# Performance work log

Measured on AMD Instinct MI355X. Metric: run time of the kernel, lower is better.

The kernel has to match this reference:

```python
import jax, jax.numpy as jnp
import numpy as np

B, N, E = 64, 256, 8192


def setup_inputs() -> dict:
    key = jax.random.key(0)
    k1, k2, k3, k4, k5 = jax.random.split(key, 5)
    P = jax.random.uniform(k1, (B, N, N), dtype=jnp.float32)
    d_error = jax.random.uniform(k2, (N, N), dtype=jnp.float32)
    edge_i = jax.random.randint(k3, (B, E), 0, N, dtype=jnp.int32)
    edge_j = jax.random.randint(k4, (B, E), 0, N, dtype=jnp.int32)
    edge_w = jax.random.uniform(k5, (B, E), dtype=jnp.float32)
    return {"P": P, "d_error": d_error, "edge_i": edge_i,
            "edge_j": edge_j, "edge_w": edge_w}


def reference(P, d_error, edge_i, edge_j, edge_w):
    # cost_e = P[b, i_e, :] @ d_error @ P[b, j_e, :]
    # Precompute Q = P @ d_error once, then gather per edge (memory-bound).
    Q = jnp.einsum('bin,nm->bim', P, d_error)            # [B, N, N]
    Qi = jnp.take_along_axis(Q, edge_i[:, :, None], axis=1)   # [B, E, N]
    Pj = jnp.take_along_axis(P, edge_j[:, :, None], axis=1)   # [B, E, N]
    cost = jnp.sum(Qi * Pj, axis=-1)                      # [B, E]
    sample_loss = jnp.sum(edge_w * cost, axis=-1)         # [B]
    sample_weight = jnp.maximum(jnp.sum(edge_w, axis=-1), 1e-8)
    # every sample has edges -> valid_samples == B, i.e. a mean over batch
    return jnp.mean(sample_loss / sample_weight)
```

## Files before the change

### kernel.cpp

```cpp
#include <hip/hip_runtime.h>

#define NN 256
#define BB 64
#define EE 8192

typedef __attribute__((ext_vector_type(8))) short bf16x8;
typedef __attribute__((ext_vector_type(8))) unsigned short u16x8;
typedef __attribute__((ext_vector_type(4))) float f32x4;

__device__ __forceinline__ unsigned short f2bf(float f) {
  union { float f; unsigned u; } x; x.f = f;
  unsigned r = x.u + 0x7FFFu + ((x.u >> 16) & 1u);
  return (unsigned short)(r >> 16);
}

__device__ __forceinline__ float bf2f(unsigned short h) {
  union { unsigned u; float f; } x; x.u = ((unsigned)h) << 16;
  return x.f;
}

__global__ __launch_bounds__(256) void convertP(const float* __restrict__ P,
                                                unsigned short* __restrict__ Pbf) {
  int idx = blockIdx.x * 256 + threadIdx.x;
  float4 v = ((const float4*)P)[idx];
  ushort4 o;
  o.x = f2bf(v.x); o.y = f2bf(v.y); o.z = f2bf(v.z); o.w = f2bf(v.w);
  ((ushort4*)Pbf)[idx] = o;
}

__global__ __launch_bounds__(256) void transposeD(const float* __restrict__ D,
                                                  unsigned short* __restrict__ Dt) {
  __shared__ float t[32][33];
  int bx = blockIdx.x & 7;
  int by = blockIdx.x >> 3;
  int c = threadIdx.x & 31, r0 = threadIdx.x >> 5;
#pragma unroll
  for (int p = 0; p < 4; ++p) {
    int row = r0 + p * 8;
    t[row][c] = D[(bx * 32 + row) * NN + by * 32 + c];
  }
  __syncthreads();
#pragma unroll
  for (int p = 0; p < 4; ++p) {
    int row = r0 + p * 8;
    Dt[(by * 32 + row) * NN + bx * 32 + c] = f2bf(t[c][row]);
  }
}

__device__ __forceinline__ void gemm_mainloop(const unsigned short* __restrict__ Ag,
                                              const unsigned short* __restrict__ Bg,
                                              int rowBase, int colBase,
                                              unsigned short* As, unsigned short* Bs,
                                              f32x4 acc[4][4]) {
  const int tid = threadIdx.x;
  const int lane = tid & 63;
  const int wave = tid >> 6;
  const int wr = (wave >> 1) * 64;
  const int wc = (wave & 1) * 64;
  const int frm = lane & 15;
  const int fq = (lane >> 4) * 8;

  for (int ks = 0; ks < 8; ++ks) {
    const int k0 = ks * 32;
    __syncthreads();
#pragma unroll
    for (int i = 0; i < 2; ++i) {
      int c = i * 256 + tid;
      int row = c >> 2;
      int col = (c & 3) * 8;
      u16x8 va = *(const u16x8*)(Ag + (rowBase + row) * NN + k0 + col);
      u16x8 vb = *(const u16x8*)(Bg + (colBase + row) * NN + k0 + col);
      *(u16x8*)(As + c * 8) = va;
      *(u16x8*)(Bs + c * 8) = vb;
    }
    __syncthreads();
    bf16x8 af[4], bfr[4];
#pragma unroll
    for (int t = 0; t < 4; ++t) {
      af[t]  = *(const bf16x8*)(As + (wr + t * 16 + frm) * 32 + fq);
      bfr[t] = *(const bf16x8*)(Bs + (wc + t * 16 + frm) * 32 + fq);
    }
#pragma unroll
    for (int tr = 0; tr < 4; ++tr)
#pragma unroll
      for (int tc = 0; tc < 4; ++tc)
        acc[tr][tc] = __builtin_amdgcn_mfma_f32_16x16x32_bf16(af[tr], bfr[tc],
                                                              acc[tr][tc], 0, 0, 0);
  }
}

__global__ __launch_bounds__(256) void gemm1(const unsigned short* __restrict__ Pbf,
                                             const unsigned short* __restrict__ Dt,
                                             unsigned short* __restrict__ Qbf) {
  __shared__ __align__(16) unsigned short As[4096];
  __shared__ __align__(16) unsigned short Bs[4096];
  int b = blockIdx.x >> 2;
  int tile = blockIdx.x & 3;
  int ty = tile >> 1, tx = tile & 1;
  f32x4 acc[4][4];
#pragma unroll
  for (int i = 0; i < 4; ++i)
#pragma unroll
    for (int j = 0; j < 4; ++j) acc[i][j] = (f32x4){0.f, 0.f, 0.f, 0.f};

  gemm_mainloop(Pbf + b * NN * NN, Dt, ty * 128, tx * 128, As, Bs, acc);

  const int lane = threadIdx.x & 63;
  const int wave = threadIdx.x >> 6;
  const int wr = (wave >> 1) * 64, wc = (wave & 1) * 64;
  unsigned short* outB = Qbf + b * NN * NN;
#pragma unroll
  for (int tr = 0; tr < 4; ++tr)
#pragma unroll
    for (int tc = 0; tc < 4; ++tc)
#pragma unroll
      for (int r = 0; r < 4; ++r) {
        int rg = ty * 128 + wr + tr * 16 + (lane >> 4) * 4 + r;
        int cg = tx * 128 + wc + tc * 16 + (lane & 15);
        outB[rg * NN + cg] = f2bf(acc[tr][tc][r]);
      }
}

__global__ __launch_bounds__(256) void gemm2_fused(const unsigned short* __restrict__ Qbf,
                                                   const unsigned short* __restrict__ Pbf,
                                                   const int* __restrict__ ei,
                                                   const int* __restrict__ ej,
                                                   const float* __restrict__ ew,
                                                   float* __restrict__ loss_part,
                                                   float* __restrict__ w_part) {
  __shared__ __align__(16) unsigned short As[4096];
  __shared__ __align__(16) unsigned short Bs[4096];
  __shared__ __align__(16) unsigned short Mt[128 * 130];
  __shared__ float red[8];
  int b = blockIdx.x >> 2;
  int tile = blockIdx.x & 3;
  int ty = tile >> 1, tx = tile & 1;
  f32x4 acc[4][4];
#pragma unroll
  for (int i = 0; i < 4; ++i)
#pragma unroll
    for (int j = 0; j < 4; ++j) acc[i][j] = (f32x4){0.f, 0.f, 0.f, 0.f};

  gemm_mainloop(Qbf + b * NN * NN, Pbf + b * NN * NN, ty * 128, tx * 128, As, Bs, acc);

  const int tid = threadIdx.x;
  const int lane = tid & 63;
  const int wave = tid >> 6;
  const int wr = (wave >> 1) * 64, wc = (wave & 1) * 64;
#pragma unroll
  for (int tr = 0; tr < 4; ++tr)
#pragma unroll
    for (int tc = 0; tc < 4; ++tc)
#pragma unroll
      for (int r = 0; r < 4; ++r) {
        int rl = wr + tr * 16 + (lane >> 4) * 4 + r;
        int cl = wc + tc * 16 + (lane & 15);
        Mt[rl * 130 + cl] = f2bf(acc[tr][tc][r]);
      }
  __syncthreads();

  float lsum = 0.f, wsum = 0.f;
  const int r0 = ty * 128, c0 = tx * 128;
  const int eb = b * EE;
#pragma unroll 4
  for (int s = 0; s < 32; ++s) {
    int e = eb + s * 256 + tid;
    int i = ei[e], j = ej[e];
    float w = ew[e];
    wsum += w;
    int il = i - r0, jl = j - c0;
    if (((unsigned)il < 128u) && ((unsigned)jl < 128u))
      lsum += w * bf2f(Mt[il * 130 + jl]);
  }
#pragma unroll
  for (int o = 32; o; o >>= 1) {
    lsum += __shfl_down(lsum, o);
    wsum += __shfl_down(wsum, o);
  }
  if (lane == 0) { red[wave] = lsum; red[4 + wave] = wsum; }
  __syncthreads();
  if (tid == 0) {
    loss_part[b * 4 + tile] = red[0] + red[1] + red[2] + red[3];
    if (tile == 0) w_part[b] = red[4] + red[5] + red[6] + red[7];
  }
}

__global__ void finalize(const float* __restrict__ loss_part,
                         const float* __restrict__ w_part,
                         float* __restrict__ out) {
  int b = threadIdx.x;
  float l = loss_part[b * 4] + loss_part[b * 4 + 1] +
            loss_part[b * 4 + 2] + loss_part[b * 4 + 3];
  float w = w_part[b];
  float r = l / fmaxf(w, 1e-8f);
#pragma unroll
  for (int o = 32; o; o >>= 1) r += __shfl_down(r, o);
  if (b == 0) out[0] = r * (1.0f / 64.0f);
}

extern "C" void kernel_launch(void* const* d_in, const int* in_sizes, int n_in,
                              void* d_out, int out_size, void* d_ws, size_t ws_size,
                              hipStream_t stream) {
  const float* P  = (const float*)d_in[0];
  const float* D  = (const float*)d_in[1];
  const int*   ei = (const int*)d_in[2];
  const int*   ej = (const int*)d_in[3];
  const float* ew = (const float*)d_in[4];
  float* out = (float*)d_out;

  char* ws = (char*)d_ws;
  unsigned short* Pbf = (unsigned short*)ws;
  unsigned short* Qbf = (unsigned short*)(ws + 8388608);
  unsigned short* Dt  = (unsigned short*)(ws + 16777216);
  float* loss_part    = (float*)(ws + 16908288);
  float* w_part       = (float*)(ws + 16909312);

  convertP<<<4096, 256, 0, stream>>>(P, Pbf);
  transposeD<<<64, 256, 0, stream>>>(D, Dt);
  gemm1<<<256, 256, 0, stream>>>(Pbf, Dt, Qbf);
  gemm2_fused<<<256, 256, 0, stream>>>(Qbf, Pbf, ei, ej, ew, loss_part, w_part);
  finalize<<<1, 64, 0, stream>>>(loss_part, w_part, out);
}
```

Before: 105.4 us.

## Fuse P bf16 conversion into GEMM loaders with register prefetch and atomic finalize

Removes the separate fp32-to-bf16 conversion kernel for P and instead converts while staging tiles in both GEMM kernels, which now read fp32 P directly. The k-loop adds register prefetching of the next tile so global loads overlap MFMA work. The finalize kernel is replaced by a per-block atomicAdd into a zeroed output, and edge loads are vectorized to int2/float2. The trade-off is reading fp32 P twice instead of bf16 P, plus nondeterministic float atomic summation order.

After: 102.5 us. -2.7%, faster.

```diff
diff --git a/kernel.cpp b/kernel.cpp
--- a/kernel.cpp
+++ b/kernel.cpp
@@ -17,15 +17,6 @@
 __device__ __forceinline__ float bf2f(unsigned short h) {
   union { unsigned u; float f; } x; x.u = ((unsigned)h) << 16;
   return x.f;
-}
-
-__global__ __launch_bounds__(256) void convertP(const float* __restrict__ P,
-                                                unsigned short* __restrict__ Pbf) {
-  int idx = blockIdx.x * 256 + threadIdx.x;
-  float4 v = ((const float4*)P)[idx];
-  ushort4 o;
-  o.x = f2bf(v.x); o.y = f2bf(v.y); o.z = f2bf(v.z); o.w = f2bf(v.w);
-  ((ushort4*)Pbf)[idx] = o;
 }
 
 __global__ __launch_bounds__(256) void transposeD(const float* __restrict__ D,
@@ -47,67 +38,78 @@
   }
 }
 
-__device__ __forceinline__ void gemm_mainloop(const unsigned short* __restrict__ Ag,
-                                              const unsigned short* __restrict__ Bg,
-                                              int rowBase, int colBase,
-                                              unsigned short* As, unsigned short* Bs,
-                                              f32x4 acc[4][4]) {
-  const int tid = threadIdx.x;
-  const int lane = tid & 63;
-  const int wave = tid >> 6;
-  const int wr = (wave >> 1) * 64;
-  const int wc = (wave & 1) * 64;
-  const int frm = lane & 15;
-  const int fq = (lane >> 4) * 8;
-
-  for (int ks = 0; ks < 8; ++ks) {
-    const int k0 = ks * 32;
-    __syncthreads();
-#pragma unroll
-    for (int i = 0; i < 2; ++i) {
-      int c = i * 256 + tid;
-      int row = c >> 2;
-      int col = (c & 3) * 8;
-      u16x8 va = *(const u16x8*)(Ag + (rowBase + row) * NN + k0 + col);
-      u16x8 vb = *(const u16x8*)(Bg + (colBase + row) * NN + k0 + col);
-      *(u16x8*)(As + c * 8) = va;
-      *(u16x8*)(Bs + c * 8) = vb;
-    }
-    __syncthreads();
-    bf16x8 af[4], bfr[4];
-#pragma unroll
-    for (int t = 0; t < 4; ++t) {
-      af[t]  = *(const bf16x8*)(As + (wr + t * 16 + frm) * 32 + fq);
-      bfr[t] = *(const bf16x8*)(Bs + (wc + t * 16 + frm) * 32 + fq);
-    }
-#pragma unroll
-    for (int tr = 0; tr < 4; ++tr)
-#pragma unroll
-      for (int tc = 0; tc < 4; ++tc)
-        acc[tr][tc] = __builtin_amdgcn_mfma_f32_16x16x32_bf16(af[tr], bfr[tc],
-                                                              acc[tr][tc], 0, 0, 0);
-  }
-}
-
-__global__ __launch_bounds__(256) void gemm1(const unsigned short* __restrict__ Pbf,
+__global__ __launch_bounds__(256) void gemm1(const float* __restrict__ P,
                                              const unsigned short* __restrict__ Dt,
                                              unsigned short* __restrict__ Qbf) {
   __shared__ __align__(16) unsigned short As[4096];
   __shared__ __align__(16) unsigned short Bs[4096];
-  int b = blockIdx.x >> 2;
-  int tile = blockIdx.x & 3;
-  int ty = tile >> 1, tx = tile & 1;
+  const int tid = threadIdx.x;
+  const int b = blockIdx.x >> 2;
+  const int tile = blockIdx.x & 3;
+  const int ty = tile >> 1, tx = tile & 1;
+  const int rowBase = ty * 128, colBase = tx * 128;
+
+  const float4* Ag4 = (const float4*)(P + b * NN * NN);
+
   f32x4 acc[4][4];
 #pragma unroll
   for (int i = 0; i < 4; ++i)
 #pragma unroll
     for (int j = 0; j < 4; ++j) acc[i][j] = (f32x4){0.f, 0.f, 0.f, 0.f};
 
-  gemm_mainloop(Pbf + b * NN * NN, Dt, ty * 128, tx * 128, As, Bs, acc);
-
-  const int lane = threadIdx.x & 63;
-  const int wave = threadIdx.x >> 6;
+  const int lane = tid & 63;
+  const int wave = tid >> 6;
   const int wr = (wave >> 1) * 64, wc = (wave & 1) * 64;
+  const int frm = lane & 15;
+  const int fq = (lane >> 4) * 8;
+
+  const int arow0 = tid >> 3, af4 = tid & 7;
+  const int brow0 = tid >> 2, bch = tid & 3;
+
+  float4 ra[4];
+  u16x8 rb[2];
+#pragma unroll
+  for (int i = 0; i < 4; ++i)
+    ra[i] = Ag4[(rowBase + arow0 + i * 32) * 64 + 0 * 8 + af4];
+#pragma unroll
+  for (int i = 0; i < 2; ++i)
+    rb[i] = *(const u16x8*)(Dt + (colBase + brow0 + i * 64) * NN + 0 * 32 + bch * 8);
+
+  for (int ks = 0; ks < 8; ++ks) {
+    __syncthreads();
+#pragma unroll
+    for (int i = 0; i < 4; ++i) {
+      ushort4 o;
+      o.x = f2bf(ra[i].x); o.y = f2bf(ra[i].y); o.z = f2bf(ra[i].z); o.w = f2bf(ra[i].w);
+      *(ushort4*)(As + (arow0 + i * 32) * 32 + af4 * 4) = o;
+    }
+#pragma unroll
+    for (int i = 0; i < 2; ++i)
+      *(u16x8*)(Bs + (brow0 + i * 64) * 32 + bch * 8) = rb[i];
+    __syncthreads();
+    if (ks < 7) {
+      const int k0 = (ks + 1) * 32;
+#pragma unroll
+      for (int i = 0; i < 4; ++i)
+        ra[i] = Ag4[(rowBase + arow0 + i * 32) * 64 + (k0 >> 2) + af4];
+#pragma unroll
+      for (int i = 0; i < 2; ++i)
+        rb[i] = *(const u16x8*)(Dt + (colBase + brow0 + i * 64) * NN + k0 + bch * 8);
+    }
+    bf16x8 af[4], bfr[4];
+#pragma unroll
+    for (int t = 0; t < 4; ++t) {
+      af[t]  = *(const bf16x8*)(As + (wr + t * 16 + frm) * 32 + fq);
+      bfr[t] = *(const bf16x8*)(Bs + (wc + t * 16 + frm) * 32 + fq);
+    }
+#pragma unroll
+    for (int tr = 0; tr < 4; ++tr)
+#pragma unroll
+      for (int tc = 0; tc < 4; ++tc)
+        acc[tr][tc] = __builtin_amdgcn_mfma_f32_16x16x32_bf16(af[tr], bfr[tc],
+                                                              acc[tr][tc], 0, 0, 0);
+  }
+
   unsigned short* outB = Qbf + b * NN * NN;
 #pragma unroll
   for (int tr = 0; tr < 4; ++tr)
@@ -115,38 +117,90 @@
     for (int tc = 0; tc < 4; ++tc)
 #pragma unroll
       for (int r = 0; r < 4; ++r) {
-        int rg = ty * 128 + wr + tr * 16 + (lane >> 4) * 4 + r;
-        int cg = tx * 128 + wc + tc * 16 + (lane & 15);
+        int rg = rowBase + wr + tr * 16 + (lane >> 4) * 4 + r;
+        int cg = colBase + wc + tc * 16 + (lane & 15);
         outB[rg * NN + cg] = f2bf(acc[tr][tc][r]);
       }
 }
 
 __global__ __launch_bounds__(256) void gemm2_fused(const unsigned short* __restrict__ Qbf,
-                                                   const unsigned short* __restrict__ Pbf,
+                                                   const float* __restrict__ P,
                                                    const int* __restrict__ ei,
                                                    const int* __restrict__ ej,
                                                    const float* __restrict__ ew,
-                                                   float* __restrict__ loss_part,
-                                                   float* __restrict__ w_part) {
+                                                   float* __restrict__ out) {
   __shared__ __align__(16) unsigned short As[4096];
   __shared__ __align__(16) unsigned short Bs[4096];
   __shared__ __align__(16) unsigned short Mt[128 * 130];
   __shared__ float red[8];
-  int b = blockIdx.x >> 2;
-  int tile = blockIdx.x & 3;
-  int ty = tile >> 1, tx = tile & 1;
+  const int tid = threadIdx.x;
+  const int b = blockIdx.x >> 2;
+  const int tile = blockIdx.x & 3;
+  const int ty = tile >> 1, tx = tile & 1;
+  const int rowBase = ty * 128, colBase = tx * 128;
+
+  const unsigned short* Ag = Qbf + b * NN * NN;
+  const float4* Bg4 = (const float4*)(P + b * NN * NN);
+
   f32x4 acc[4][4];
 #pragma unroll
   for (int i = 0; i < 4; ++i)
 #pragma unroll
     for (int j = 0; j < 4; ++j) acc[i][j] = (f32x4){0.f, 0.f, 0.f, 0.f};
 
-  gemm_mainloop(Qbf + b * NN * NN, Pbf + b * NN * NN, ty * 128, tx * 128, As, Bs, acc);
-
-  const int tid = threadIdx.x;
   const int lane = tid & 63;
   const int wave = tid >> 6;
   const int wr = (wave >> 1) * 64, wc = (wave & 1) * 64;
+  const int frm = lane & 15;
+  const int fq = (lane >> 4) * 8;
+
+  const int arow0 = tid >> 2, ach = tid & 3;
+  const int brow0 = tid >> 3, bf4 = tid & 7;
+
+  u16x8 ra[2];
+  float4 rb[4];
+#pragma unroll
+  for (int i = 0; i < 2; ++i)
+    ra[i] = *(const u16x8*)(Ag + (rowBase + arow0 + i * 64) * NN + ach * 8);
+#pragma unroll
+  for (int i = 0; i < 4; ++i)
+    rb[i] = Bg4[(colBase + brow0 + i * 32) * 64 + bf4];
+
+  for (int ks = 0; ks < 8; ++ks) {
+    __syncthreads();
+#pragma unroll
+    for (int i = 0; i < 2; ++i)
+      *(u16x8*)(As + (arow0 + i * 64) * 32 + ach * 8) = ra[i];
+#pragma unroll
+    for (int i = 0; i < 4; ++i) {
+      ushort4 o;
+      o.x = f2bf(rb[i].x); o.y = f2bf(rb[i].y); o.z = f2bf(rb[i].z); o.w = f2bf(rb[i].w);
+      *(ushort4*)(Bs + (brow0 + i * 32) * 32 + bf4 * 4) = o;
+    }
+    __syncthreads();
+    if (ks < 7) {
+      const int k0 = (ks + 1) * 32;
+#pragma unroll
+      for (int i = 0; i < 2; ++i)
+        ra[i] = *(const u16x8*)(Ag + (rowBase + arow0 + i * 64) * NN + k0 + ach * 8);
+#pragma unroll
+      for (int i = 0; i < 4; ++i)
+        rb[i] = Bg4[(colBase + brow0 + i * 32) * 64 + (k0 >> 2) + bf4];
+    }
+    bf16x8 af[4], bfr[4];
+#pragma unroll
+    for (int t = 0; t < 4; ++t) {
+      af[t]  = *(const bf16x8*)(As + (wr + t * 16 + frm) * 32 + fq);
+      bfr[t] = *(const bf16x8*)(Bs + (wc + t * 16 + frm) * 32 + fq);
+    }
+#pragma unroll
+    for (int tr = 0; tr < 4; ++tr)
+#pragma unroll
+      for (int tc = 0; tc < 4; ++tc)
+        acc[tr][tc] = __builtin_amdgcn_mfma_f32_16x16x32_bf16(af[tr], bfr[tc],
+                                                              acc[tr][tc], 0, 0, 0);
+  }
+
 #pragma unroll
   for (int tr = 0; tr < 4; ++tr)
 #pragma unroll
@@ -160,17 +214,22 @@
   __syncthreads();
 
   float lsum = 0.f, wsum = 0.f;
-  const int r0 = ty * 128, c0 = tx * 128;
-  const int eb = b * EE;
+  const int2*   ei2 = (const int2*)(ei + b * EE);
+  const int2*   ej2 = (const int2*)(ej + b * EE);
+  const float2* ew2 = (const float2*)(ew + b * EE);
 #pragma unroll 4
-  for (int s = 0; s < 32; ++s) {
-    int e = eb + s * 256 + tid;
-    int i = ei[e], j = ej[e];
-    float w = ew[e];
-    wsum += w;
-    int il = i - r0, jl = j - c0;
+  for (int s = 0; s < 16; ++s) {
+    int idx = s * 256 + tid;
+    int2 ii = ei2[idx];
+    int2 jj = ej2[idx];
+    float2 ww = ew2[idx];
+    wsum += ww.x + ww.y;
+    int il = ii.x - rowBase, jl = jj.x - colBase;
     if (((unsigned)il < 128u) && ((unsigned)jl < 128u))
-      lsum += w * bf2f(Mt[il * 130 + jl]);
+      lsum += ww.x * bf2f(Mt[il * 130 + jl]);
+    il = ii.y - rowBase; jl = jj.y - colBase;
+    if (((unsigned)il < 128u) && ((unsigned)jl < 128u))
+      lsum += ww.y * bf2f(Mt[il * 130 + jl]);
   }
 #pragma unroll
   for (int o = 32; o; o >>= 1) {
@@ -180,22 +239,10 @@
   if (lane == 0) { red[wave] = lsum; red[4 + wave] = wsum; }
   __syncthreads();
   if (tid == 0) {
-    loss_part[b * 4 + tile] = red[0] + red[1] + red[2] + red[3];
-    if (tile == 0) w_part[b] = red[4] + red[5] + red[6] + red[7];
-  }
-}
-
-__global__ void finalize(const float* __restrict__ loss_part,
-                         const float* __restrict__ w_part,
-                         float* __restrict__ out) {
-  int b = threadIdx.x;
-  float l = loss_part[b * 4] + loss_part[b * 4 + 1] +
-            loss_part[b * 4 + 2] + loss_part[b * 4 + 3];
-  float w = w_part[b];
-  float r = l / fmaxf(w, 1e-8f);
-#pragma unroll
-  for (int o = 32; o; o >>= 1) r += __shfl_down(r, o);
-  if (b == 0) out[0] = r * (1.0f / 64.0f);
+    float l = red[0] + red[1] + red[2] + red[3];
+    float w = red[4] + red[5] + red[6] + red[7];
+    atomicAdd(out, l / (64.0f * fmaxf(w, 1e-8f)));
+  }
 }
 
 extern "C" void kernel_launch(void* const* d_in, const int* in_sizes, int n_in,
@@ -209,15 +256,11 @@
   float* out = (float*)d_out;
 
   char* ws = (char*)d_ws;
-  unsigned short* Pbf = (unsigned short*)ws;
-  unsigned short* Qbf = (unsigned short*)(ws + 8388608);
-  unsigned short* Dt  = (unsigned short*)(ws + 16777216);
-  float* loss_part    = (float*)(ws + 16908288);
-  float* w_part       = (float*)(ws + 16909312);
-
-  convertP<<<4096, 256, 0, stream>>>(P, Pbf);
+  unsigned short* Qbf = (unsigned short*)ws;
+  unsigned short* Dt  = (unsigned short*)(ws + 8388608);
+
+  hipMemsetAsync(out, 0, out_size * sizeof(float), stream);
   transposeD<<<64, 256, 0, stream>>>(D, Dt);
-  gemm1<<<256, 256, 0, stream>>>(Pbf, Dt, Qbf);
-  gemm2_fused<<<256, 256, 0, stream>>>(Qbf, Pbf, ei, ej, ew, loss_part, w_part);
-  finalize<<<1, 64, 0, stream>>>(loss_part, w_part, out);
-}
+  gemm1<<<256, 256, 0, stream>>>(P, Dt, Qbf);
+  gemm2_fused<<<256, 256, 0, stream>>>(Qbf, P, ei, ej, ew, out);
+}
```
